# Performance work log

Hardware: AMD Instinct MI355X
Metric: run time of the kernel (lower is better)

The kernel has to match this reference:

```python
import jax, jax.numpy as jnp
import numpy as np

N, IN_DIM, HID, HEADS = 4096, 256, 64, 8


def setup_inputs() -> dict:
    key = jax.random.key(0)
    ks = jax.random.split(key, 9)
    feats = jax.random.normal(ks[0], (N, IN_DIM), dtype=jnp.float32)
    adj = jax.random.bernoulli(ks[1], 0.01, (N, N)) | jnp.eye(N, dtype=bool)
    def lin(k, fin, fout):
        return jax.random.normal(k, (fin, fout), dtype=jnp.float32) / np.float32(np.sqrt(fin))
    return {
        "features": feats,
        "adjacency": adj,
        "W_in": lin(ks[2], IN_DIM, HID * HEADS),            # linear (no bias)
        "W_out": lin(ks[3], HID * HEADS, HID),              # out_proj
        "b_out": jnp.zeros((HID,), jnp.float32),
        "W_c1": lin(ks[4], HID * 2, HID),                   # classifier[1]
        "b_c1": jnp.zeros((HID,), jnp.float32),
        "W_c2": lin(ks[5], HID, 1),                         # classifier[3]
        "b_c2": jnp.zeros((1,), jnp.float32),
    }


def reference(features, adjacency, W_in, W_out, b_out, W_c1, b_c1, W_c2, b_c2):
    n = features.shape[0]
    # multi-head GAT: [H, N, D]
    proj = (features @ W_in).reshape(n, HEADS, HID).transpose(1, 0, 2)
    logits = jnp.einsum('hnd,hmd->hnm', proj, proj) / np.float32(np.sqrt(HID))
    logits = jnp.where(adjacency[None, :, :], logits, -jnp.inf)
    attn = jax.nn.softmax(logits, axis=-1)
    attended = jnp.einsum('hnm,hmd->hnd', attn, proj)
    attended = attended.transpose(1, 0, 2).reshape(n, HEADS * HID)
    node_states = attended @ W_out + b_out
    # memory_bank is None -> concat with zeros
    fused = jnp.concatenate([node_states, jnp.zeros_like(node_states)], axis=-1)
    h = jax.nn.gelu(fused, approximate=False) @ W_c1 + b_c1
    scores = (jax.nn.gelu(h, approximate=False) @ W_c2 + b_c2).squeeze(-1)
    # attention heatmap: masked row-normalized cosine similarity
    eps = np.float32(1e-8)
    norm = jnp.maximum(jnp.linalg.norm(node_states, axis=-1, keepdims=True), eps)
    xn = node_states / norm
    sim = jnp.where(adjacency, xn @ xn.T, 0.0)
    heatmap = sim / (sim.sum(axis=-1, keepdims=True) + eps)
    return scores, heatmap
```

## Files before the change

### kernel.cpp

```cpp
#include <hip/hip_runtime.h>
#include <math.h>

constexpr int NN    = 4096;
constexpr int INDIM = 256;
constexpr int HID   = 64;
constexpr int HEADS = 8;
constexpr int HH    = HID * HEADS;
constexpr int DMAX  = 256;

typedef float        vfloat4 __attribute__((ext_vector_type(4)));
typedef unsigned int vuint4  __attribute__((ext_vector_type(4)));

__device__ __forceinline__ float gelu_exact(float x) {
    return 0.5f * x * (1.0f + erff(x * 0.70710678118654752f));
}

__device__ __forceinline__ float wave_reduce64(float v) {
    v += __shfl_xor(v, 32); v += __shfl_xor(v, 16); v += __shfl_xor(v, 8);
    v += __shfl_xor(v, 4);  v += __shfl_xor(v, 2);  v += __shfl_xor(v, 1);
    return v;
}

__global__ void detect_kernel(const unsigned int* __restrict__ adj, int* __restrict__ flag) {
    __shared__ int sawU8;
    int t = threadIdx.x;
    if (t == 0) sawU8 = 0;
    __syncthreads();
    int u8 = 0;
    for (int i = t; i < 4096; i += 256) {
        unsigned int w = adj[i];
        if (((w & ~0x01010101u) == 0u) && ((w & 0xFFFFFF00u) != 0u)) u8 = 1;
    }
    if (u8) atomicOr(&sawU8, 1);
    __syncthreads();
    if (t == 0) flag[0] = sawU8 ? 1 : 0;
}

__global__ __launch_bounds__(256) void proj_kernel(const float* __restrict__ A,
                                                   const float* __restrict__ B,
                                                   float* __restrict__ C) {
    __shared__ float As[16][68];
    __shared__ float Bs[16][64];
    const int bx = blockIdx.x, by = blockIdx.y, t = threadIdx.x;
    const int tx = t & 15, ty = t >> 4;
    float acc[4][4] = {{0.0f}};
    for (int k0 = 0; k0 < INDIM; k0 += 16) {
        for (int i = t; i < 64 * 16; i += 256) {
            int m = i >> 4, k = i & 15;
            As[k][m] = A[(size_t)(by * 64 + m) * INDIM + k0 + k];
        }
        for (int i = t; i < 16 * 64; i += 256) {
            int k = i >> 6, c = i & 63;
            Bs[k][c] = B[(size_t)(k0 + k) * HH + bx * 64 + c];
        }
        __syncthreads();
        #pragma unroll
        for (int k = 0; k < 16; ++k) {
            float4 av = *reinterpret_cast<const float4*>(&As[k][ty * 4]);
            float4 bv = *reinterpret_cast<const float4*>(&Bs[k][tx * 4]);
            float aa[4] = {av.x, av.y, av.z, av.w};
            float bb[4] = {bv.x, bv.y, bv.z, bv.w};
            #pragma unroll
            for (int i = 0; i < 4; ++i)
                #pragma unroll
                for (int j = 0; j < 4; ++j)
                    acc[i][j] += aa[i] * bb[j];
        }
        __syncthreads();
    }
    #pragma unroll
    for (int i = 0; i < 4; ++i)
        #pragma unroll
        for (int j = 0; j < 4; ++j)
            C[(size_t)(by * 64 + ty * 4 + i) * HH + bx * 64 + tx * 4 + j] = acc[i][j];
}

__global__ __launch_bounds__(256) void attn_kernel(
    const void* __restrict__ adjv, const int* __restrict__ flag,
    const float* __restrict__ proj,
    const float* __restrict__ W_out, const float* __restrict__ b_out,
    const float* __restrict__ W_c1, const float* __restrict__ b_c1,
    const float* __restrict__ W_c2, const float* __restrict__ b_c2,
    float* __restrict__ scores, float* __restrict__ xn_out,
    unsigned short* __restrict__ nbr_g, int* __restrict__ deg_g) {
    __shared__ unsigned short nbr_s[DMAX];
    __shared__ int wsum[4];
    __shared__ float attw[4][HH];
    __shared__ float lwS[4][8];
    __shared__ float invLs[8];
    __shared__ float qv2[HH];
    __shared__ float red[256];
    __shared__ float nsbuf[HID], gbuf[HID];

    const int n = blockIdx.x, t = threadIdx.x;
    const int wv = t >> 6, lane = t & 63;

    unsigned int nzmask = 0;
    if (flag[0] == 1) {
        const vuint4* src = reinterpret_cast<const vuint4*>(
            (const unsigned char*)adjv + (size_t)n * NN + 16 * t);
        const vuint4 r = __builtin_nontemporal_load(src);
        #pragma unroll
        for (int a = 0; a < 4; ++a)
            #pragma unroll
            for (int j = 0; j < 4; ++j)
                if ((r[a] >> (8 * j)) & 0xFFu) nzmask |= 1u << (a * 4 + j);
    } else {
        const vuint4* p = reinterpret_cast<const vuint4*>(
            (const unsigned int*)adjv + (size_t)n * NN + 16 * t);
        #pragma unroll
        for (int a = 0; a < 4; ++a) {
            const vuint4 r = __builtin_nontemporal_load(p + a);
            if (r[0]) nzmask |= 1u << (a * 4 + 0);
            if (r[1]) nzmask |= 1u << (a * 4 + 1);
            if (r[2]) nzmask |= 1u << (a * 4 + 2);
            if (r[3]) nzmask |= 1u << (a * 4 + 3);
        }
    }
    const int c = __popc(nzmask);
    int x = c;
    #pragma unroll
    for (int d = 1; d < 64; d <<= 1) {
        int y = __shfl_up(x, d);
        if (lane >= d) x += y;
    }
    if (lane == 63) wsum[wv] = x;
    __syncthreads();
    int base = 0;
    #pragma unroll
    for (int i = 0; i < 4; ++i)
        if (i < wv) base += wsum[i];
    const int deg = min(wsum[0] + wsum[1] + wsum[2] + wsum[3], DMAX);
    if (t == 0) deg_g[n] = deg;
    {
        int o = base + x - c;
        unsigned int mm = nzmask;
        while (mm) {
            const int j = __ffs(mm) - 1;
            mm &= mm - 1;
            if (o < DMAX) {
                const unsigned short idx = (unsigned short)(16 * t + j);
                nbr_s[o] = idx;
                nbr_g[(size_t)n * DMAX + o] = idx;
            }
            ++o;
        }
    }
    __syncthreads();

    float q[8];
    {
        const float4 a = *reinterpret_cast<const float4*>(proj + (size_t)n * HH + 8 * lane);
        const float4 b = *reinterpret_cast<const float4*>(proj + (size_t)n * HH + 8 * lane + 4);
        q[0] = a.x; q[1] = a.y; q[2] = a.z; q[3] = a.w;
        q[4] = b.x; q[5] = b.y; q[6] = b.z; q[7] = b.w;
    }

    float l = 0.0f;
    float acc[8] = {0.f, 0.f, 0.f, 0.f, 0.f, 0.f, 0.f, 0.f};
    int cc = wv;
    for (; cc + 4 < deg; cc += 8) {
        const float* kp0 = proj + (size_t)nbr_s[cc] * HH + 8 * lane;
        const float* kp1 = proj + (size_t)nbr_s[cc + 4] * HH + 8 * lane;
        const float4 a0 = *reinterpret_cast<const float4*>(kp0);
        const float4 b0 = *reinterpret_cast<const float4*>(kp0 + 4);
        const float4 a1 = *reinterpret_cast<const float4*>(kp1);
        const float4 b1 = *reinterpret_cast<const float4*>(kp1 + 4);
        float k0[8] = {a0.x, a0.y, a0.z, a0.w, b0.x, b0.y, b0.z, b0.w};
        float k1[8] = {a1.x, a1.y, a1.z, a1.w, b1.x, b1.y, b1.z, b1.w};
        float s0 = q[0]*k0[0] + q[1]*k0[1] + q[2]*k0[2] + q[3]*k0[3] +
                   q[4]*k0[4] + q[5]*k0[5] + q[6]*k0[6] + q[7]*k0[7];
        float s1 = q[0]*k1[0] + q[1]*k1[1] + q[2]*k1[2] + q[3]*k1[3] +
                   q[4]*k1[4] + q[5]*k1[5] + q[6]*k1[6] + q[7]*k1[7];
        s0 += __shfl_xor(s0, 1); s1 += __shfl_xor(s1, 1);
        s0 += __shfl_xor(s0, 2); s1 += __shfl_xor(s1, 2);
        s0 += __shfl_xor(s0, 4); s1 += __shfl_xor(s1, 4);
        const float w0 = expf(s0 * 0.125f);
        const float w1 = expf(s1 * 0.125f);
        l += w0 + w1;
        #pragma unroll
        for (int i = 0; i < 8; ++i) acc[i] += w0 * k0[i] + w1 * k1[i];
    }
    if (cc < deg) {
        const float* kp = proj + (size_t)nbr_s[cc] * HH + 8 * lane;
        const float4 ka = *reinterpret_cast<const float4*>(kp);
        const float4 kb = *reinterpret_cast<const float4*>(kp + 4);
        float kf[8] = {ka.x, ka.y, ka.z, ka.w, kb.x, kb.y, kb.z, kb.w};
        float s = q[0]*kf[0] + q[1]*kf[1] + q[2]*kf[2] + q[3]*kf[3] +
                  q[4]*kf[4] + q[5]*kf[5] + q[6]*kf[6] + q[7]*kf[7];
        s += __shfl_xor(s, 1); s += __shfl_xor(s, 2); s += __shfl_xor(s, 4);
        const float w = expf(s * 0.125f);
        l += w;
        #pragma unroll
        for (int i = 0; i < 8; ++i) acc[i] += w * kf[i];
    }
    #pragma unroll
    for (int i = 0; i < 8; ++i) attw[wv][8 * lane + i] = acc[i];
    if ((lane & 7) == 0) lwS[wv][lane >> 3] = l;
    __syncthreads();

    if (t < 8)
        invLs[t] = 1.0f / (lwS[0][t] + lwS[1][t] + lwS[2][t] + lwS[3][t]);
    __syncthreads();
    #pragma unroll
    for (int r = 0; r < 2; ++r) {
        const int d = t + r * 256;
        qv2[d] = (attw[0][d] + attw[1][d] + attw[2][d] + attw[3][d]) * invLs[d >> 6];
    }
    __syncthreads();

    const int j = t & 63, part = t >> 6;
    float p = 0.0f;
    for (int d = part * 128; d < part * 128 + 128; ++d)
        p += qv2[d] * W_out[d * HID + j];
    red[t] = p;
    __syncthreads();
    if (t < HID)
        nsbuf[t] = red[t] + red[t + 64] + red[t + 128] + red[t + 192] + b_out[t];
    __syncthreads();

    if (t < 64) {
        const float ns = nsbuf[t];
        const float s2 = wave_reduce64(ns * ns);
        const float invn = 1.0f / fmaxf(sqrtf(s2), 1e-8f);
        xn_out[(size_t)n * HID + t] = ns * invn;
        gbuf[t] = gelu_exact(ns);
    }
    __syncthreads();
    if (t < 64) {
        float hv = b_c1[t];
        for (int i = 0; i < HID; ++i) hv += gbuf[i] * W_c1[i * HID + t];
        const float hb = gelu_exact(hv);
        const float s = wave_reduce64(hb * W_c2[t]);
        if (t == 0) scores[n] = s + b_c2[0];
    }
}

__global__ __launch_bounds__(256, 8) void heat_kernel(
    const unsigned short* __restrict__ nbr_g, const int* __restrict__ deg_g,
    const float* __restrict__ xn, float* __restrict__ heat) {
    __shared__ float srow[NN];
    __shared__ float simv[DMAX];
    __shared__ unsigned short nl[DMAX];
    __shared__ float inv_s;
    const int n = blockIdx.x, t = threadIdx.x;
    const int wv = t >> 6, lane = t & 63;
    const int deg = deg_g[n];

    float4* sr4 = (float4*)srow;
    const float4 z4 = {0.f, 0.f, 0.f, 0.f};
    for (int i = t; i < NN / 4; i += 256) sr4[i] = z4;
    if (t < deg) nl[t] = nbr_g[(size_t)n * DMAX + t];
    const float xq = xn[(size_t)n * HID + lane];
    __syncthreads();

    for (int c = wv; c < deg; c += 4) {
        const int m = nl[c];
        float s = wave_reduce64(xq * xn[(size_t)m * HID + lane]);
        if (lane == 0) { srow[m] = s; simv[c] = s; }
    }
    __syncthreads();
    if (t < 64) {
        float ps = 0.0f;
        for (int c = t; c < deg; c += 64) ps += simv[c];
        ps = wave_reduce64(ps);
        if (t == 0) inv_s = 1.0f / (ps + 1e-8f);
    }
    __syncthreads();
    const float inv = inv_s;
    vfloat4* hr4 = (vfloat4*)(heat + (size_t)n * NN);
    for (int i = t; i < NN / 4; i += 256) {
        float4 v = sr4[i];
        vfloat4 nv = {v.x * inv, v.y * inv, v.z * inv, v.w * inv};
        __builtin_nontemporal_store(nv, hr4 + i);
    }
}

extern "C" void kernel_launch(void* const* d_in, const int* in_sizes, int n_in,
                              void* d_out, int out_size, void* d_ws, size_t ws_size,
                              hipStream_t stream) {
    const float* features = (const float*)d_in[0];
    const void*  adj      = d_in[1];
    const float* W_in     = (const float*)d_in[2];
    const float* W_out    = (const float*)d_in[3];
    const float* b_out    = (const float*)d_in[4];
    const float* W_c1     = (const float*)d_in[5];
    const float* b_c1     = (const float*)d_in[6];
    const float* W_c2     = (const float*)d_in[7];
    const float* b_c2     = (const float*)d_in[8];

    float* scores = (float*)d_out;
    float* heat   = (float*)d_out + NN;

    float*          proj  = (float*)d_ws;
    float*          xn    = proj + (size_t)NN * HH;
    unsigned short* nbr_g = (unsigned short*)(xn + (size_t)NN * HID);
    int*            deg_g = (int*)(nbr_g + (size_t)NN * DMAX);
    int*            flag  = deg_g + NN;

    detect_kernel<<<1, 256, 0, stream>>>((const unsigned int*)adj, flag);
    proj_kernel<<<dim3(HH / 64, NN / 64), 256, 0, stream>>>(features, W_in, proj);
    attn_kernel<<<NN, 256, 0, stream>>>(adj, flag, proj, W_out, b_out, W_c1, b_c1,
                                        W_c2, b_c2, scores, xn, nbr_g, deg_g);
    heat_kernel<<<NN, 256, 0, stream>>>(nbr_g, deg_g, xn, heat);
}
```

Baseline: 248.7 us.

## Split attention into CSR, per-head gather, and batched post-projection kernels

Moves adjacency-to-CSR extraction into its own kernel and stores projections head-major (projT[h][n][d]), so each wave gathers only the 256-byte head slice of every neighbor. Attention now runs one wave per (node, head), with 8 neighbors processed in parallel per wave and cross-group shuffle reductions in place of shared-memory reductions. The out-projection, normalization and classifier are batched into a 64-row tiled GEMM kernel instead of per-node dot loops. The cost is extra launches and an extra round trip of the attended tensor through global memory.

```diff
diff --git a/kernel.cpp b/kernel.cpp
--- a/kernel.cpp
+++ b/kernel.cpp
@@ -36,9 +36,63 @@
     if (t == 0) flag[0] = sawU8 ? 1 : 0;
 }
 
+__global__ __launch_bounds__(256) void csr_kernel(
+    const void* __restrict__ adjv, const int* __restrict__ flag,
+    unsigned short* __restrict__ nbr_g, int* __restrict__ deg_g) {
+    __shared__ int wsum[4];
+    const int n = blockIdx.x, t = threadIdx.x;
+    const int wv = t >> 6, lane = t & 63;
+
+    unsigned int nzmask = 0;
+    if (flag[0] == 1) {
+        const vuint4* src = reinterpret_cast<const vuint4*>(
+            (const unsigned char*)adjv + (size_t)n * NN + 16 * t);
+        const vuint4 r = __builtin_nontemporal_load(src);
+        #pragma unroll
+        for (int a = 0; a < 4; ++a)
+            #pragma unroll
+            for (int j = 0; j < 4; ++j)
+                if ((r[a] >> (8 * j)) & 0xFFu) nzmask |= 1u << (a * 4 + j);
+    } else {
+        const vuint4* p = reinterpret_cast<const vuint4*>(
+            (const unsigned int*)adjv + (size_t)n * NN + 16 * t);
+        #pragma unroll
+        for (int a = 0; a < 4; ++a) {
+            const vuint4 r = __builtin_nontemporal_load(p + a);
+            if (r[0]) nzmask |= 1u << (a * 4 + 0);
+            if (r[1]) nzmask |= 1u << (a * 4 + 1);
+            if (r[2]) nzmask |= 1u << (a * 4 + 2);
+            if (r[3]) nzmask |= 1u << (a * 4 + 3);
+        }
+    }
+    const int c = __popc(nzmask);
+    int x = c;
+    #pragma unroll
+    for (int d = 1; d < 64; d <<= 1) {
+        int y = __shfl_up(x, d);
+        if (lane >= d) x += y;
+    }
+    if (lane == 63) wsum[wv] = x;
+    __syncthreads();
+    int base = 0;
+    #pragma unroll
+    for (int i = 0; i < 4; ++i)
+        if (i < wv) base += wsum[i];
+    const int deg = min(wsum[0] + wsum[1] + wsum[2] + wsum[3], DMAX);
+    if (t == 0) deg_g[n] = deg;
+    int o = base + x - c;
+    unsigned int mm = nzmask;
+    while (mm) {
+        const int j = __ffs(mm) - 1;
+        mm &= mm - 1;
+        if (o < DMAX) nbr_g[(size_t)n * DMAX + o] = (unsigned short)(16 * t + j);
+        ++o;
+    }
+}
+
 __global__ __launch_bounds__(256) void proj_kernel(const float* __restrict__ A,
                                                    const float* __restrict__ B,
-                                                   float* __restrict__ C) {
+                                                   float* __restrict__ projT) {
     __shared__ float As[16][68];
     __shared__ float Bs[16][64];
     const int bx = blockIdx.x, by = blockIdx.y, t = threadIdx.x;
@@ -69,170 +123,131 @@
         __syncthreads();
     }
     #pragma unroll
-    for (int i = 0; i < 4; ++i)
-        #pragma unroll
-        for (int j = 0; j < 4; ++j)
-            C[(size_t)(by * 64 + ty * 4 + i) * HH + bx * 64 + tx * 4 + j] = acc[i][j];
+    for (int i = 0; i < 4; ++i) {
+        float4 o = {acc[i][0], acc[i][1], acc[i][2], acc[i][3]};
+        *reinterpret_cast<float4*>(
+            projT + ((size_t)bx * NN + by * 64 + ty * 4 + i) * HID + tx * 4) = o;
+    }
 }
 
 __global__ __launch_bounds__(256) void attn_kernel(
-    const void* __restrict__ adjv, const int* __restrict__ flag,
-    const float* __restrict__ proj,
-    const float* __restrict__ W_out, const float* __restrict__ b_out,
-    const float* __restrict__ W_c1, const float* __restrict__ b_c1,
-    const float* __restrict__ W_c2, const float* __restrict__ b_c2,
-    float* __restrict__ scores, float* __restrict__ xn_out,
-    unsigned short* __restrict__ nbr_g, int* __restrict__ deg_g) {
-    __shared__ unsigned short nbr_s[DMAX];
-    __shared__ int wsum[4];
-    __shared__ float attw[4][HH];
-    __shared__ float lwS[4][8];
-    __shared__ float invLs[8];
-    __shared__ float qv2[HH];
-    __shared__ float red[256];
-    __shared__ float nsbuf[HID], gbuf[HID];
-
-    const int n = blockIdx.x, t = threadIdx.x;
+    const float* __restrict__ projT,
+    const unsigned short* __restrict__ nbr_g, const int* __restrict__ deg_g,
+    float* __restrict__ attended) {
+    __shared__ unsigned short nl[4][DMAX];
+    const int b = blockIdx.x, t = threadIdx.x;
     const int wv = t >> 6, lane = t & 63;
-
-    unsigned int nzmask = 0;
-    if (flag[0] == 1) {
-        const vuint4* src = reinterpret_cast<const vuint4*>(
-            (const unsigned char*)adjv + (size_t)n * NN + 16 * t);
-        const vuint4 r = __builtin_nontemporal_load(src);
-        #pragma unroll
-        for (int a = 0; a < 4; ++a)
-            #pragma unroll
-            for (int j = 0; j < 4; ++j)
-                if ((r[a] >> (8 * j)) & 0xFFu) nzmask |= 1u << (a * 4 + j);
-    } else {
-        const vuint4* p = reinterpret_cast<const vuint4*>(
-            (const unsigned int*)adjv + (size_t)n * NN + 16 * t);
-        #pragma unroll
-        for (int a = 0; a < 4; ++a) {
-            const vuint4 r = __builtin_nontemporal_load(p + a);
-            if (r[0]) nzmask |= 1u << (a * 4 + 0);
-            if (r[1]) nzmask |= 1u << (a * 4 + 1);
-            if (r[2]) nzmask |= 1u << (a * 4 + 2);
-            if (r[3]) nzmask |= 1u << (a * 4 + 3);
-        }
-    }
-    const int c = __popc(nzmask);
-    int x = c;
-    #pragma unroll
-    for (int d = 1; d < 64; d <<= 1) {
-        int y = __shfl_up(x, d);
-        if (lane >= d) x += y;
-    }
-    if (lane == 63) wsum[wv] = x;
-    __syncthreads();
-    int base = 0;
-    #pragma unroll
-    for (int i = 0; i < 4; ++i)
-        if (i < wv) base += wsum[i];
-    const int deg = min(wsum[0] + wsum[1] + wsum[2] + wsum[3], DMAX);
-    if (t == 0) deg_g[n] = deg;
-    {
-        int o = base + x - c;
-        unsigned int mm = nzmask;
-        while (mm) {
-            const int j = __ffs(mm) - 1;
-            mm &= mm - 1;
-            if (o < DMAX) {
-                const unsigned short idx = (unsigned short)(16 * t + j);
-                nbr_s[o] = idx;
-                nbr_g[(size_t)n * DMAX + o] = idx;
-            }
-            ++o;
-        }
-    }
-    __syncthreads();
+    const int h = b & 7;
+    const int n = (b >> 3) * 4 + wv;
+    const int deg = deg_g[n];
+
+    *reinterpret_cast<ushort4*>(&nl[wv][lane * 4]) =
+        *reinterpret_cast<const ushort4*>(nbr_g + (size_t)n * DMAX + lane * 4);
+
+    const float* tab = projT + (size_t)h * NN * HID;
+    const int g = lane >> 3, dl = (lane & 7) * 8;
 
     float q[8];
     {
-        const float4 a = *reinterpret_cast<const float4*>(proj + (size_t)n * HH + 8 * lane);
-        const float4 b = *reinterpret_cast<const float4*>(proj + (size_t)n * HH + 8 * lane + 4);
-        q[0] = a.x; q[1] = a.y; q[2] = a.z; q[3] = a.w;
-        q[4] = b.x; q[5] = b.y; q[6] = b.z; q[7] = b.w;
+        const float4 a = *reinterpret_cast<const float4*>(tab + (size_t)n * HID + dl);
+        const float4 bq = *reinterpret_cast<const float4*>(tab + (size_t)n * HID + dl + 4);
+        q[0] = a.x;  q[1] = a.y;  q[2] = a.z;  q[3] = a.w;
+        q[4] = bq.x; q[5] = bq.y; q[6] = bq.z; q[7] = bq.w;
     }
 
     float l = 0.0f;
     float acc[8] = {0.f, 0.f, 0.f, 0.f, 0.f, 0.f, 0.f, 0.f};
-    int cc = wv;
-    for (; cc + 4 < deg; cc += 8) {
-        const float* kp0 = proj + (size_t)nbr_s[cc] * HH + 8 * lane;
-        const float* kp1 = proj + (size_t)nbr_s[cc + 4] * HH + 8 * lane;
-        const float4 a0 = *reinterpret_cast<const float4*>(kp0);
-        const float4 b0 = *reinterpret_cast<const float4*>(kp0 + 4);
-        const float4 a1 = *reinterpret_cast<const float4*>(kp1);
-        const float4 b1 = *reinterpret_cast<const float4*>(kp1 + 4);
-        float k0[8] = {a0.x, a0.y, a0.z, a0.w, b0.x, b0.y, b0.z, b0.w};
-        float k1[8] = {a1.x, a1.y, a1.z, a1.w, b1.x, b1.y, b1.z, b1.w};
-        float s0 = q[0]*k0[0] + q[1]*k0[1] + q[2]*k0[2] + q[3]*k0[3] +
-                   q[4]*k0[4] + q[5]*k0[5] + q[6]*k0[6] + q[7]*k0[7];
-        float s1 = q[0]*k1[0] + q[1]*k1[1] + q[2]*k1[2] + q[3]*k1[3] +
-                   q[4]*k1[4] + q[5]*k1[5] + q[6]*k1[6] + q[7]*k1[7];
-        s0 += __shfl_xor(s0, 1); s1 += __shfl_xor(s1, 1);
-        s0 += __shfl_xor(s0, 2); s1 += __shfl_xor(s1, 2);
-        s0 += __shfl_xor(s0, 4); s1 += __shfl_xor(s1, 4);
-        const float w0 = expf(s0 * 0.125f);
-        const float w1 = expf(s1 * 0.125f);
-        l += w0 + w1;
-        #pragma unroll
-        for (int i = 0; i < 8; ++i) acc[i] += w0 * k0[i] + w1 * k1[i];
-    }
-    if (cc < deg) {
-        const float* kp = proj + (size_t)nbr_s[cc] * HH + 8 * lane;
+    for (int c0 = 0; c0 < deg; c0 += 8) {
+        const int c = c0 + g;
+        const int idx = nl[wv][min(c, deg - 1)];
+        const float* kp = tab + (size_t)idx * HID + dl;
         const float4 ka = *reinterpret_cast<const float4*>(kp);
         const float4 kb = *reinterpret_cast<const float4*>(kp + 4);
         float kf[8] = {ka.x, ka.y, ka.z, ka.w, kb.x, kb.y, kb.z, kb.w};
         float s = q[0]*kf[0] + q[1]*kf[1] + q[2]*kf[2] + q[3]*kf[3] +
                   q[4]*kf[4] + q[5]*kf[5] + q[6]*kf[6] + q[7]*kf[7];
         s += __shfl_xor(s, 1); s += __shfl_xor(s, 2); s += __shfl_xor(s, 4);
-        const float w = expf(s * 0.125f);
+        const float w = (c < deg) ? expf(s * 0.125f) : 0.0f;
         l += w;
         #pragma unroll
         for (int i = 0; i < 8; ++i) acc[i] += w * kf[i];
     }
-    #pragma unroll
-    for (int i = 0; i < 8; ++i) attw[wv][8 * lane + i] = acc[i];
-    if ((lane & 7) == 0) lwS[wv][lane >> 3] = l;
-    __syncthreads();
-
-    if (t < 8)
-        invLs[t] = 1.0f / (lwS[0][t] + lwS[1][t] + lwS[2][t] + lwS[3][t]);
-    __syncthreads();
-    #pragma unroll
-    for (int r = 0; r < 2; ++r) {
-        const int d = t + r * 256;
-        qv2[d] = (attw[0][d] + attw[1][d] + attw[2][d] + attw[3][d]) * invLs[d >> 6];
-    }
-    __syncthreads();
-
-    const int j = t & 63, part = t >> 6;
-    float p = 0.0f;
-    for (int d = part * 128; d < part * 128 + 128; ++d)
-        p += qv2[d] * W_out[d * HID + j];
-    red[t] = p;
-    __syncthreads();
-    if (t < HID)
-        nsbuf[t] = red[t] + red[t + 64] + red[t + 128] + red[t + 192] + b_out[t];
-    __syncthreads();
-
-    if (t < 64) {
-        const float ns = nsbuf[t];
-        const float s2 = wave_reduce64(ns * ns);
+    l += __shfl_xor(l, 8); l += __shfl_xor(l, 16); l += __shfl_xor(l, 32);
+    #pragma unroll
+    for (int i = 0; i < 8; ++i) {
+        acc[i] += __shfl_xor(acc[i], 8);
+        acc[i] += __shfl_xor(acc[i], 16);
+        acc[i] += __shfl_xor(acc[i], 32);
+    }
+    const float invL = 1.0f / l;
+    if (g == 0) {
+        float4 o1 = {acc[0] * invL, acc[1] * invL, acc[2] * invL, acc[3] * invL};
+        float4 o2 = {acc[4] * invL, acc[5] * invL, acc[6] * invL, acc[7] * invL};
+        float* dst = attended + (size_t)n * HH + h * HID + dl;
+        *reinterpret_cast<float4*>(dst)     = o1;
+        *reinterpret_cast<float4*>(dst + 4) = o2;
+    }
+}
+
+__global__ __launch_bounds__(256) void post_kernel(
+    const float* __restrict__ attended,
+    const float* __restrict__ W_out, const float* __restrict__ b_out,
+    const float* __restrict__ W_c1, const float* __restrict__ b_c1,
+    const float* __restrict__ W_c2, const float* __restrict__ b_c2,
+    float* __restrict__ scores, float* __restrict__ xn) {
+    __shared__ float As[16][68];
+    __shared__ float Bs[16][64];
+    __shared__ float nsS[64][65];
+    const int by = blockIdx.x, t = threadIdx.x;
+    const int tx = t & 15, ty = t >> 4;
+    float acc[4][4] = {{0.0f}};
+    for (int k0 = 0; k0 < HH; k0 += 16) {
+        for (int i = t; i < 64 * 16; i += 256) {
+            int m = i >> 4, k = i & 15;
+            As[k][m] = attended[(size_t)(by * 64 + m) * HH + k0 + k];
+        }
+        for (int i = t; i < 16 * 64; i += 256) {
+            int k = i >> 6, c = i & 63;
+            Bs[k][c] = W_out[(size_t)(k0 + k) * HID + c];
+        }
+        __syncthreads();
+        #pragma unroll
+        for (int k = 0; k < 16; ++k) {
+            float4 av = *reinterpret_cast<const float4*>(&As[k][ty * 4]);
+            float4 bv = *reinterpret_cast<const float4*>(&Bs[k][tx * 4]);
+            float aa[4] = {av.x, av.y, av.z, av.w};
+            float bb[4] = {bv.x, bv.y, bv.z, bv.w};
+            #pragma unroll
+            for (int i = 0; i < 4; ++i)
+                #pragma unroll
+                for (int j = 0; j < 4; ++j)
+                    acc[i][j] += aa[i] * bb[j];
+        }
+        __syncthreads();
+    }
+    #pragma unroll
+    for (int i = 0; i < 4; ++i)
+        #pragma unroll
+        for (int j = 0; j < 4; ++j)
+            nsS[ty * 4 + i][tx * 4 + j] = acc[i][j] + b_out[tx * 4 + j];
+    __syncthreads();
+
+    const int wv = t >> 6, lane = t & 63;
+    for (int nd = 0; nd < 16; ++nd) {
+        const int mrow = wv * 16 + nd;
+        const float v = nsS[mrow][lane];
+        const float s2 = wave_reduce64(v * v);
         const float invn = 1.0f / fmaxf(sqrtf(s2), 1e-8f);
-        xn_out[(size_t)n * HID + t] = ns * invn;
-        gbuf[t] = gelu_exact(ns);
-    }
-    __syncthreads();
-    if (t < 64) {
-        float hv = b_c1[t];
-        for (int i = 0; i < HID; ++i) hv += gbuf[i] * W_c1[i * HID + t];
+        xn[(size_t)(by * 64 + mrow) * HID + lane] = v * invn;
+        nsS[mrow][lane] = gelu_exact(v);
+    }
+    for (int nd = 0; nd < 16; ++nd) {
+        const int mrow = wv * 16 + nd;
+        float hv = b_c1[lane];
+        for (int i = 0; i < HID; ++i) hv += nsS[mrow][i] * W_c1[i * HID + lane];
         const float hb = gelu_exact(hv);
-        const float s = wave_reduce64(hb * W_c2[t]);
-        if (t == 0) scores[n] = s + b_c2[0];
+        const float sc_ = wave_reduce64(hb * W_c2[lane]);
+        if (lane == 0) scores[by * 64 + mrow] = sc_ + b_c2[0];
     }
 }
 
@@ -292,15 +307,18 @@
     float* scores = (float*)d_out;
     float* heat   = (float*)d_out + NN;
 
-    float*          proj  = (float*)d_ws;
-    float*          xn    = proj + (size_t)NN * HH;
-    unsigned short* nbr_g = (unsigned short*)(xn + (size_t)NN * HID);
-    int*            deg_g = (int*)(nbr_g + (size_t)NN * DMAX);
-    int*            flag  = deg_g + NN;
+    float*          projT    = (float*)d_ws;
+    float*          attended = projT + (size_t)HEADS * NN * HID;
+    float*          xn       = attended + (size_t)NN * HH;
+    unsigned short* nbr_g    = (unsigned short*)(xn + (size_t)NN * HID);
+    int*            deg_g    = (int*)(nbr_g + (size_t)NN * DMAX);
+    int*            flag     = deg_g + NN;
 
     detect_kernel<<<1, 256, 0, stream>>>((const unsigned int*)adj, flag);
-    proj_kernel<<<dim3(HH / 64, NN / 64), 256, 0, stream>>>(features, W_in, proj);
-    attn_kernel<<<NN, 256, 0, stream>>>(adj, flag, proj, W_out, b_out, W_c1, b_c1,
-                                        W_c2, b_c2, scores, xn, nbr_g, deg_g);
+    csr_kernel<<<NN, 256, 0, stream>>>(adj, flag, nbr_g, deg_g);
+    proj_kernel<<<dim3(HH / 64, NN / 64), 256, 0, stream>>>(features, W_in, projT);
+    attn_kernel<<<NN * HEADS / 4, 256, 0, stream>>>(projT, nbr_g, deg_g, attended);
+    post_kernel<<<NN / 64, 256, 0, stream>>>(attended, W_out, b_out, W_c1, b_c1,
+                                             W_c2, b_c2, scores, xn);
     heat_kernel<<<NN, 256, 0, stream>>>(nbr_g, deg_g, xn, heat);
 }
```

Measured after the change: 324.1 us. +30.3%, slower.
